# Kernel tuning notes

Hardware: AMD Instinct MI355X
Metric: run time of the kernel (lower is better)

Reference implementation:

```python
import jax, jax.numpy as jnp
import numpy as np

NUM_PATCHES = 16
FILTER_SIZE = 4
IN_CHANNELS = 64
OUT_CHANNELS = 256
BATCH = 64


def setup_inputs() -> dict:
    key = jax.random.key(0)
    k1, k2 = jax.random.split(key)
    D = NUM_PATCHES * FILTER_SIZE
    x = jax.random.normal(k1, (BATCH, IN_CHANNELS, D, D), dtype=jnp.float32)
    w = jax.random.normal(
        k2,
        (OUT_CHANNELS, IN_CHANNELS, NUM_PATCHES, NUM_PATCHES, FILTER_SIZE ** 2),
        dtype=jnp.float32,
    )
    return {"x": x, "w": w}


def reference(x, w):
    # x: (N, C, D, D) with D = P*f ; w: (O, C, P, P, f^2)
    N, C, D, _ = x.shape
    O, _, P, _, f2 = w.shape
    f = int(round(f2 ** 0.5))
    # non-overlapping unfold: (N,C,P,f,P,f) -> (N,C,P,P,f,f) -> (N,C,P,P,f^2)
    patches = x.reshape(N, C, P, f, P, f).transpose(0, 1, 2, 4, 3, 5).reshape(N, C, P, P, f2)
    # locally-connected contraction over in_channels and filter elements
    y = jnp.einsum('ncpqf,ocpqf->nopq', patches, w)
    scale = 1.0 / jnp.sqrt(jnp.asarray(f2 * C, dtype=x.dtype))
    return jax.nn.relu(y * scale)
```

## Files before the change

kernel.cpp:

```cpp
#include <hip/hip_runtime.h>


typedef float    f32x4 __attribute__((ext_vector_type(4)));
typedef _Float16 f16x4 __attribute__((ext_vector_type(4)));

__device__ __forceinline__ void gload16(const void* g, void* l) {
    __builtin_amdgcn_global_load_lds(
        (const __attribute__((address_space(1))) void*)g,
        (__attribute__((address_space(3))) void*)l, 16, 0, 0);
}

__device__ __forceinline__ f16x4 cvt4(f32x4 v) {
    f16x4 r;
    r[0] = (_Float16)v[0]; r[1] = (_Float16)v[1];
    r[2] = (_Float16)v[2]; r[3] = (_Float16)v[3];
    return r;
}

__global__ __launch_bounds__(512)
void locblock_fused(const float* __restrict__ x, const float* __restrict__ w,
                    float* __restrict__ out) {
    __shared__ __align__(16) char smem[131072];

    const int hw = blockIdx.x;
    const int lb = (hw & 7) * 32 + (hw >> 3);
    const int p  = lb >> 4;
    const int q4 = (lb >> 2) & 3;
    const int oq = lb & 3;

    const int tid  = (int)threadIdx.x;
    const int lane = tid & 63;
    const int l15  = lane & 15;
    const int kq   = lane >> 4;
    const int wv   = tid >> 6;
    const int qiw  = wv >> 1;
    const int ow   = wv & 1;

    const float* xsrc[2];
#pragma unroll
    for (int j = 0; j < 2; ++j) {
        const int id = j * 512 + tid;
        const int n = id >> 4, s = id & 15;
        const int u = s ^ (n & 15);
        xsrc[j] = x + (size_t)n * 262144u
                    + (size_t)(4 * p + (u >> 2)) * 64u
                    + (size_t)(q4 * 16 + (u & 3) * 4);
    }
    const float* wsrc[2];
#pragma unroll
    for (int j = 0; j < 2; ++j) {
        const int id = j * 512 + tid;
        const int o = id >> 4, s = id & 15;
        const int u = s ^ (o & 15);
        wsrc[j] = w + (size_t)(oq * 64 + o) * 262144u
                    + (size_t)p * 256u + (size_t)(q4 * 64)
                    + (size_t)((u >> 2) * 16 + (u & 3) * 4);
    }

    int aoff[4], boff[2];
#pragma unroll
    for (int mf = 0; mf < 4; ++mf)
        aoff[mf] = (mf * 16 + l15) * 256 + (((kq * 4 + qiw) ^ l15) * 16);
#pragma unroll
    for (int nf = 0; nf < 2; ++nf)
        boff[nf] = 16384 + (ow * 32 + nf * 16 + l15) * 256
                 + (((qiw * 4 + kq) ^ l15) * 16);

    f32x4 acc[4][2];
#pragma unroll
    for (int mf = 0; mf < 4; ++mf)
#pragma unroll
        for (int nf = 0; nf < 2; ++nf)
            acc[mf][nf] = (f32x4){0.f, 0.f, 0.f, 0.f};

    auto stage = [&](int c) {
        char* base = smem + (size_t)(c & 3) * 32768u;
        const size_t coff = (size_t)c * 4096u;
#pragma unroll
        for (int j = 0; j < 2; ++j)
            gload16(xsrc[j] + coff, base + j * 8192 + tid * 16);
#pragma unroll
        for (int j = 0; j < 2; ++j)
            gload16(wsrc[j] + coff, base + 16384 + j * 8192 + tid * 16);
    };

    auto compute = [&](int c) {
        const char* Lb = smem + (size_t)(c & 3) * 32768u;
        f16x4 av[4], bv[2];
#pragma unroll
        for (int mf = 0; mf < 4; ++mf)
            av[mf] = cvt4(*(const f32x4*)(Lb + aoff[mf]));
#pragma unroll
        for (int nf = 0; nf < 2; ++nf)
            bv[nf] = cvt4(*(const f32x4*)(Lb + boff[nf]));
#pragma unroll
        for (int mf = 0; mf < 4; ++mf)
#pragma unroll
            for (int nf = 0; nf < 2; ++nf)
                acc[mf][nf] = __builtin_amdgcn_mfma_f32_16x16x16f16(
                    av[mf], bv[nf], acc[mf][nf], 0, 0, 0);
    };

    stage(0);
    stage(1);
    stage(2);
#pragma unroll 1
    for (int t = 0; t < 61; ++t) {
        asm volatile("s_waitcnt vmcnt(8)" ::: "memory");
        __builtin_amdgcn_s_barrier();
        stage(t + 3);
        compute(t);
    }
    asm volatile("s_waitcnt vmcnt(8)" ::: "memory");
    __builtin_amdgcn_s_barrier();
    compute(61);
    asm volatile("s_waitcnt vmcnt(4)" ::: "memory");
    __builtin_amdgcn_s_barrier();
    compute(62);
    asm volatile("s_waitcnt vmcnt(0)" ::: "memory");
    __builtin_amdgcn_s_barrier();
    compute(63);

    __syncthreads();

    float* T = (float*)smem;
    const float scale = 0.03125f;
#pragma unroll
    for (int mf = 0; mf < 4; ++mf)
#pragma unroll
        for (int nf = 0; nf < 2; ++nf) {
            const int o  = ow * 32 + nf * 16 + l15;
            const int n0 = mf * 16 + kq * 4;
            f32x4 r;
#pragma unroll
            for (int j = 0; j < 4; ++j)
                r[j] = fmaxf(acc[mf][nf][j] * scale, 0.0f);
            *(f32x4*)(T + (size_t)(qiw * 64 + o) * 72u + n0) = r;
        }
    __syncthreads();

#pragma unroll
    for (int i = 0; i < 8; ++i) {
        const int item = i * 512 + tid;
        const int n = item >> 6, o = item & 63;
        f32x4 r;
#pragma unroll
        for (int s = 0; s < 4; ++s)
            r[s] = T[(size_t)(s * 64 + o) * 72u + n];
        *(f32x4*)(out + (size_t)n * 65536u + (size_t)(oq * 64 + o) * 256u
                      + (size_t)(p * 16 + q4 * 4)) = r;
    }
}

extern "C" void kernel_launch(void* const* d_in, const int* in_sizes, int n_in,
                              void* d_out, int out_size, void* d_ws, size_t ws_size,
                              hipStream_t stream) {
    const float* x = (const float*)d_in[0];
    const float* w = (const float*)d_in[1];
    float* out = (float*)d_out;
    locblock_fused<<<dim3(256), dim3(512), 0, stream>>>(x, w, out);
}
```

Measured before the change: 85.41 us.

## Retile blocks to 2 patch columns by 128 outputs to cut x reloads

Changes each block's work tile from 4 patch columns by 64 output channels to 2 patch columns by 128 output channels. The point is to halve how many blocks re-read each x patch, which cuts global input traffic, while total weight traffic stays the same. Each pipeline stage now issues three async loads instead of four, and the LDS ring buffer shrinks accordingly, with vmcnt waits adjusted to match. The epilogue now writes 8-byte vectors instead of 16-byte ones, which may hurt store efficiency.

```diff
diff --git a/kernel.cpp b/kernel.cpp
--- a/kernel.cpp
+++ b/kernel.cpp
@@ -2,6 +2,7 @@
 
 
 typedef float    f32x4 __attribute__((ext_vector_type(4)));
+typedef float    f32x2 __attribute__((ext_vector_type(2)));
 typedef _Float16 f16x4 __attribute__((ext_vector_type(4)));
 
 __device__ __forceinline__ void gload16(const void* g, void* l) {
@@ -20,51 +21,45 @@
 __global__ __launch_bounds__(512)
 void locblock_fused(const float* __restrict__ x, const float* __restrict__ w,
                     float* __restrict__ out) {
-    __shared__ __align__(16) char smem[131072];
+    __shared__ __align__(16) char smem[98304];
 
     const int hw = blockIdx.x;
     const int lb = (hw & 7) * 32 + (hw >> 3);
     const int p  = lb >> 4;
-    const int q4 = (lb >> 2) & 3;
-    const int oq = lb & 3;
+    const int q2 = (lb >> 1) & 7;
+    const int oh = lb & 1;
 
     const int tid  = (int)threadIdx.x;
     const int lane = tid & 63;
     const int l15  = lane & 15;
     const int kq   = lane >> 4;
     const int wv   = tid >> 6;
-    const int qiw  = wv >> 1;
-    const int ow   = wv & 1;
+    const int qw   = wv & 1;
+    const int nc   = wv >> 1;
 
-    const float* xsrc[2];
-#pragma unroll
-    for (int j = 0; j < 2; ++j) {
-        const int id = j * 512 + tid;
-        const int n = id >> 4, s = id & 15;
-        const int u = s ^ (n & 15);
-        xsrc[j] = x + (size_t)n * 262144u
-                    + (size_t)(4 * p + (u >> 2)) * 64u
-                    + (size_t)(q4 * 16 + (u & 3) * 4);
-    }
+    const int xn = tid >> 3, xs = tid & 7;
+    const int xu = xs ^ (xn & 7);
+    const float* xsrc = x + (size_t)xn * 262144u
+                          + (size_t)(4 * p + (xu >> 1)) * 64u
+                          + (size_t)(q2 * 8 + (xu & 1) * 4);
     const float* wsrc[2];
 #pragma unroll
     for (int j = 0; j < 2; ++j) {
         const int id = j * 512 + tid;
-        const int o = id >> 4, s = id & 15;
-        const int u = s ^ (o & 15);
-        wsrc[j] = w + (size_t)(oq * 64 + o) * 262144u
-                    + (size_t)p * 256u + (size_t)(q4 * 64)
-                    + (size_t)((u >> 2) * 16 + (u & 3) * 4);
+        const int o = id >> 3, s = id & 7;
+        const int u = s ^ (o & 7);
+        wsrc[j] = w + (size_t)(oh * 128 + o) * 262144u
+                    + (size_t)p * 256u + (size_t)(q2 * 32) + (size_t)(u * 4);
     }
 
     int aoff[4], boff[2];
 #pragma unroll
     for (int mf = 0; mf < 4; ++mf)
-        aoff[mf] = (mf * 16 + l15) * 256 + (((kq * 4 + qiw) ^ l15) * 16);
+        aoff[mf] = (mf * 16 + l15) * 128 + (((kq * 2 + qw) ^ (l15 & 7)) * 16);
 #pragma unroll
     for (int nf = 0; nf < 2; ++nf)
-        boff[nf] = 16384 + (ow * 32 + nf * 16 + l15) * 256
-                 + (((qiw * 4 + kq) ^ l15) * 16);
+        boff[nf] = 8192 + (nc * 32 + nf * 16 + l15) * 128
+                 + (((qw * 4 + kq) ^ (l15 & 7)) * 16);
 
     f32x4 acc[4][2];
 #pragma unroll
@@ -74,18 +69,16 @@
             acc[mf][nf] = (f32x4){0.f, 0.f, 0.f, 0.f};
 
     auto stage = [&](int c) {
-        char* base = smem + (size_t)(c & 3) * 32768u;
+        char* base = smem + (size_t)(c & 3) * 24576u;
         const size_t coff = (size_t)c * 4096u;
+        gload16(xsrc + coff, base + tid * 16);
 #pragma unroll
         for (int j = 0; j < 2; ++j)
-            gload16(xsrc[j] + coff, base + j * 8192 + tid * 16);
-#pragma unroll
-        for (int j = 0; j < 2; ++j)
-            gload16(wsrc[j] + coff, base + 16384 + j * 8192 + tid * 16);
+            gload16(wsrc[j] + coff, base + 8192 + j * 8192 + tid * 16);
     };
 
     auto compute = [&](int c) {
-        const char* Lb = smem + (size_t)(c & 3) * 32768u;
+        const char* Lb = smem + (size_t)(c & 3) * 24576u;
         f16x4 av[4], bv[2];
 #pragma unroll
         for (int mf = 0; mf < 4; ++mf)
@@ -106,15 +99,15 @@
     stage(2);
 #pragma unroll 1
     for (int t = 0; t < 61; ++t) {
-        asm volatile("s_waitcnt vmcnt(8)" ::: "memory");
+        asm volatile("s_waitcnt vmcnt(6)" ::: "memory");
         __builtin_amdgcn_s_barrier();
         stage(t + 3);
         compute(t);
     }
-    asm volatile("s_waitcnt vmcnt(8)" ::: "memory");
+    asm volatile("s_waitcnt vmcnt(6)" ::: "memory");
     __builtin_amdgcn_s_barrier();
     compute(61);
-    asm volatile("s_waitcnt vmcnt(4)" ::: "memory");
+    asm volatile("s_waitcnt vmcnt(3)" ::: "memory");
     __builtin_amdgcn_s_barrier();
     compute(62);
     asm volatile("s_waitcnt vmcnt(0)" ::: "memory");
@@ -129,26 +122,25 @@
     for (int mf = 0; mf < 4; ++mf)
 #pragma unroll
         for (int nf = 0; nf < 2; ++nf) {
-            const int o  = ow * 32 + nf * 16 + l15;
+            const int o  = nc * 32 + nf * 16 + l15;
             const int n0 = mf * 16 + kq * 4;
             f32x4 r;
 #pragma unroll
             for (int j = 0; j < 4; ++j)
                 r[j] = fmaxf(acc[mf][nf][j] * scale, 0.0f);
-            *(f32x4*)(T + (size_t)(qiw * 64 + o) * 72u + n0) = r;
+            *(f32x4*)(T + (size_t)(qw * 128 + o) * 72u + n0) = r;
         }
     __syncthreads();
 
 #pragma unroll
-    for (int i = 0; i < 8; ++i) {
+    for (int i = 0; i < 16; ++i) {
         const int item = i * 512 + tid;
-        const int n = item >> 6, o = item & 63;
-        f32x4 r;
-#pragma unroll
-        for (int s = 0; s < 4; ++s)
-            r[s] = T[(size_t)(s * 64 + o) * 72u + n];
-        *(f32x4*)(out + (size_t)n * 65536u + (size_t)(oq * 64 + o) * 256u
-                      + (size_t)(p * 16 + q4 * 4)) = r;
+        const int n = item & 63, o = (item >> 6) & 127;
+        f32x2 r;
+        r[0] = T[(size_t)o * 72u + n];
+        r[1] = T[(size_t)(128 + o) * 72u + n];
+        *(f32x2*)(out + (size_t)n * 65536u + (size_t)(oh * 128 + o) * 256u
+                      + (size_t)(p * 16 + q2 * 2)) = r;
     }
 }
 
```

Result: slower. 92.72 us (+8.6%).
